# Optimization experiments

Hardware: AMD Instinct MI355X
Metric: run time of the kernel (lower is better)

## Reference

```python
import jax, jax.numpy as jnp
import numpy as np

G, N, E, C = 4, 50000, 800000, 128


def setup_inputs() -> dict:
    key = jax.random.key(0)
    ks = jax.random.split(key, 8)
    x = jax.random.normal(ks[0], (G, N, C), dtype=jnp.float32)
    edge_index = jax.random.randint(ks[1], (G, 2, E), 0, N, dtype=jnp.int64)
    s = 1.0 / np.sqrt(C)
    W1 = jax.random.normal(ks[2], (G, C, C), dtype=jnp.float32) * s
    W2 = jax.random.normal(ks[3], (G, C, C), dtype=jnp.float32) * s
    W3 = jax.random.normal(ks[4], (G, C, C), dtype=jnp.float32) * s
    b1 = jnp.zeros((G, C), dtype=jnp.float32)
    b2 = jnp.zeros((G, C), dtype=jnp.float32)
    b3 = jnp.zeros((G, C), dtype=jnp.float32)
    return {"x": x, "edge_index": edge_index, "W1": W1, "b1": b1,
            "W2": W2, "b2": b2, "W3": W3, "b3": b3}


def _gcn_layer(x, src, dst, deg_inv_sqrt, W, b):
    # PyG GCNConv: linear, then D^-1/2 (A+I) D^-1/2 aggregation, then bias.
    h = x @ W                                   # [N, C_out]
    norm = deg_inv_sqrt[src] * deg_inv_sqrt[dst]  # [E+N]
    msg = h[src] * norm[:, None]                # gather + scale
    out = jax.ops.segment_sum(msg, dst, num_segments=x.shape[0])
    return out + b


def _forward_one(x, ei, W1, b1, W2, b2, W3, b3):
    n = x.shape[0]
    loops = jnp.arange(n, dtype=ei.dtype)
    src = jnp.concatenate([ei[0], loops])       # add self-loops
    dst = jnp.concatenate([ei[1], loops])
    deg = jax.ops.segment_sum(jnp.ones_like(src, dtype=x.dtype), dst, num_segments=n)
    dis = jnp.where(deg > 0, jax.lax.rsqrt(deg), 0.0)
    x = _gcn_layer(x, src, dst, dis, W1, b1)
    x = _gcn_layer(x, src, dst, dis, W2, b2)
    x = _gcn_layer(x, src, dst, dis, W3, b3)
    return x


def reference(x, edge_index, W1, b1, W2, b2, W3, b3):
    # vmap over the num_graphs independent GCN stacks, then concat node dim
    out = jax.vmap(_forward_one)(x, edge_index, W1, b1, W2, b2, W3, b3)
    return out.reshape(-1, out.shape[-1])       # [G*N, out_channels]
```

## Files before the change

kernel.cpp:

```cpp
#include <hip/hip_runtime.h>

#define NG 4
#define NN 50000
#define NE 800000
#define NC 128
#define NB 196
#define NBT (NG * NB)
#define CAPB 48
#define LBS (NB + 1)
#define CAPQ 4608

typedef _Float16 half8 __attribute__((ext_vector_type(8)));
typedef _Float16 half4 __attribute__((ext_vector_type(4)));
typedef float f32x4 __attribute__((ext_vector_type(4)));

__global__ __launch_bounds__(256) void init_cursors(int* __restrict__ bktCur) {
  int i = blockIdx.x * blockDim.x + threadIdx.x;
  if (i < NBT) bktCur[i] = i * CAPQ;
}

__global__ __launch_bounds__(256) void bucket_scatter(
    const int* __restrict__ ei, int* __restrict__ bktCur,
    unsigned int* __restrict__ rec) {
  __shared__ int lcnt[NB];
  __shared__ int lbase[NB];
  __shared__ unsigned int lbin[CAPB * LBS];
  int g = blockIdx.y;
  int tid = threadIdx.x;
  for (int i = tid; i < NB; i += 256) lcnt[i] = 0;
  __syncthreads();
  const int* srcp = ei + (size_t)g * 2 * NE;
  const int* dstp = srcp + NE;
  int e0 = blockIdx.x * 4096;
  for (int t = tid; t < 4096; t += 256) {
    int e = e0 + t;
    if (e < NE) {
      int s = srcp[e], d = dstp[e];
      int b = d >> 8;
      unsigned int r = ((unsigned int)(d & 255) << 16) | (unsigned int)s;
      int pos = atomicAdd(&lcnt[b], 1);
      if (pos < CAPB) lbin[pos * LBS + b] = r;
      else { int gp = atomicAdd(&bktCur[g * NB + b], 1); rec[gp] = r; }
    }
  }
  __syncthreads();
  if (tid < NB) {
    int n = lcnt[tid]; if (n > CAPB) n = CAPB;
    lbase[tid] = n ? atomicAdd(&bktCur[g * NB + tid], n) : 0;
  }
  __syncthreads();
  int lane = tid & 63, wv = tid >> 6;
  for (int b = wv; b < NB; b += 4) {
    int n = lcnt[b]; if (n > CAPB) n = CAPB;
    if (lane < n) rec[lbase[b] + lane] = lbin[lane * LBS + b];
  }
}

__global__ __launch_bounds__(256) void build_csr(
    const unsigned int* __restrict__ rec, const int* __restrict__ bktCur,
    unsigned short* __restrict__ col, int* __restrict__ off,
    unsigned short* __restrict__ deg, float* __restrict__ dis) {
  __shared__ int cnt[256];
  __shared__ int offv[256];
  __shared__ int cnt2[256];
  __shared__ int wsum[4];
  int g = blockIdx.y, b = blockIdx.x;
  int idx = g * NB + b;
  int rb = idx * CAPQ, re = bktCur[idx];
  int tid = threadIdx.x;
  cnt[tid] = 0;
  __syncthreads();
  for (int j = rb + tid; j < re; j += 256)
    atomicAdd(&cnt[(rec[j] >> 16) & 255], 1);
  __syncthreads();
  int lane = tid & 63, wv = tid >> 6;
  int v = cnt[tid], incl = v;
  #pragma unroll
  for (int d2 = 1; d2 < 64; d2 <<= 1) {
    int t = __shfl_up(incl, d2, 64);
    if (lane >= d2) incl += t;
  }
  if (lane == 63) wsum[wv] = incl;
  __syncthreads();
  if (tid == 0) {
    int s = 0;
    #pragma unroll
    for (int w = 0; w < 4; ++w) { int t = wsum[w]; wsum[w] = s; s += t; }
  }
  __syncthreads();
  int excl = wsum[wv] + incl - v;
  offv[tid] = excl;
  cnt2[tid] = 0;
  int node = b * 256 + tid;
  if (node < NN) {
    off[g * (NN + 1) + node] = rb + excl;
    deg[(size_t)g * NN + node] = (unsigned short)v;
    dis[(size_t)g * NN + node] = rsqrtf((float)(v + 1));
  }
  __syncthreads();
  for (int j = rb + tid; j < re; j += 256) {
    unsigned int r = rec[j];
    int dl = (r >> 16) & 255;
    int p = rb + offv[dl] + atomicAdd(&cnt2[dl], 1);
    col[p] = (unsigned short)(r & 0xFFFF);
  }
}

__global__ __launch_bounds__(256) void gemm_mfma_kernel(
    const float* __restrict__ x, const float* __restrict__ W,
    const float* __restrict__ dis, _Float16* __restrict__ h) {
  __shared__ _Float16 Wt[2][128 * 128];
  int g = blockIdx.y;
  int row0 = blockIdx.x * 128;
  int tid = threadIdx.x;
  int lane = tid & 63;
  int wv = tid >> 6;
  int kc = lane >> 4;
  int lr = lane & 15;
  const float* Wg = W + (size_t)g * NC * NC;
  const float* xg = x + (size_t)g * NN * NC;

  {
    int n = tid & 127;
    int kq = (tid >> 7) & 1;
    #pragma unroll
    for (int iter = 0; iter < 16; ++iter) {
      int k4 = iter * 8 + kq * 4;
      float w0 = Wg[(size_t)(k4 + 0) * NC + n];
      float w1 = Wg[(size_t)(k4 + 1) * NC + n];
      float w2 = Wg[(size_t)(k4 + 2) * NC + n];
      float w3 = Wg[(size_t)(k4 + 3) * NC + n];
      half4 hi, lo;
      hi[0] = (_Float16)w0; lo[0] = (_Float16)(w0 - (float)hi[0]);
      hi[1] = (_Float16)w1; lo[1] = (_Float16)(w1 - (float)hi[1]);
      hi[2] = (_Float16)w2; lo[2] = (_Float16)(w2 - (float)hi[2]);
      hi[3] = (_Float16)w3; lo[3] = (_Float16)(w3 - (float)hi[3]);
      int base = n * 128 + ((iter ^ (n & 15)) << 3) + kq * 4;
      *(half4*)&Wt[0][base] = hi;
      *(half4*)&Wt[1][base] = lo;
    }
  }
  __syncthreads();

  f32x4 acc[2][8];
  #pragma unroll
  for (int mb = 0; mb < 2; ++mb)
    #pragma unroll
    for (int nb = 0; nb < 8; ++nb)
      acc[mb][nb] = (f32x4){0.f, 0.f, 0.f, 0.f};

  for (int kstep = 0; kstep < 4; ++kstep) {
    half8 ah[2], al[2];
    #pragma unroll
    for (int mb = 0; mb < 2; ++mb) {
      int row = row0 + wv * 32 + mb * 16 + lr;
      if (row > NN - 1) row = NN - 1;
      const float* xp = xg + (size_t)row * NC + kstep * 32 + kc * 8;
      float4 v0 = *(const float4*)xp;
      float4 v1 = *(const float4*)(xp + 4);
      float vv0 = v0.x, vv1 = v0.y, vv2 = v0.z, vv3 = v0.w;
      float vv4 = v1.x, vv5 = v1.y, vv6 = v1.z, vv7 = v1.w;
      _Float16 t;
      t = (_Float16)vv0; ah[mb][0] = t; al[mb][0] = (_Float16)(vv0 - (float)t);
      t = (_Float16)vv1; ah[mb][1] = t; al[mb][1] = (_Float16)(vv1 - (float)t);
      t = (_Float16)vv2; ah[mb][2] = t; al[mb][2] = (_Float16)(vv2 - (float)t);
      t = (_Float16)vv3; ah[mb][3] = t; al[mb][3] = (_Float16)(vv3 - (float)t);
      t = (_Float16)vv4; ah[mb][4] = t; al[mb][4] = (_Float16)(vv4 - (float)t);
      t = (_Float16)vv5; ah[mb][5] = t; al[mb][5] = (_Float16)(vv5 - (float)t);
      t = (_Float16)vv6; ah[mb][6] = t; al[mb][6] = (_Float16)(vv6 - (float)t);
      t = (_Float16)vv7; ah[mb][7] = t; al[mb][7] = (_Float16)(vv7 - (float)t);
    }
    #pragma unroll
    for (int nb = 0; nb < 8; ++nb) {
      int n = nb * 16 + lr;
      int chunk = kstep * 4 + kc;
      int boff = n * 128 + ((chunk ^ (n & 15)) << 3);
      half8 bh = *(const half8*)&Wt[0][boff];
      half8 bl = *(const half8*)&Wt[1][boff];
      #pragma unroll
      for (int mb = 0; mb < 2; ++mb) {
        acc[mb][nb] = __builtin_amdgcn_mfma_f32_16x16x32_f16(ah[mb], bh, acc[mb][nb], 0, 0, 0);
        acc[mb][nb] = __builtin_amdgcn_mfma_f32_16x16x32_f16(al[mb], bh, acc[mb][nb], 0, 0, 0);
        acc[mb][nb] = __builtin_amdgcn_mfma_f32_16x16x32_f16(ah[mb], bl, acc[mb][nb], 0, 0, 0);
      }
    }
  }

  const float* disg = dis + (size_t)g * NN;
  _Float16* hg = h + (size_t)g * NN * NC;
  #pragma unroll
  for (int mb = 0; mb < 2; ++mb) {
    #pragma unroll
    for (int reg = 0; reg < 4; ++reg) {
      int row = row0 + wv * 32 + mb * 16 + kc * 4 + reg;
      if (row < NN) {
        float dsc = disg[row];
        half8 o;
        #pragma unroll
        for (int nb = 0; nb < 8; ++nb)
          o[nb] = (_Float16)(acc[mb][nb][reg] * dsc);
        *(half8*)(hg + (size_t)row * NC + lr * 8) = o;
      }
    }
  }
}

#define MIXACC(A, H) A = fmaf((float)(H), 1.0f, A)
__global__ __launch_bounds__(256) void agg_kernel(
    const _Float16* __restrict__ h, const int* __restrict__ off,
    const unsigned short* __restrict__ col, const unsigned short* __restrict__ deg,
    const float* __restrict__ dis, const float* __restrict__ b,
    float* __restrict__ out) {
  int bid = blockIdx.x;
  int g = (bid & 7) >> 1;
  int sub = ((bid >> 3) << 1) | (bid & 1);
  int node = sub * 16 + (threadIdx.x >> 4);
  if (sub >= NN / 16) return;
  int l = threadIdx.x & 15;
  const half8* h8 = (const half8*)(h + (size_t)g * NN * NC);
  float a0[8], a1[8], a2[8], a3[8];
  half8 v = h8[(size_t)node * 16 + l];
  #pragma unroll
  for (int i = 0; i < 8; ++i) {
    a0[i] = (float)v[i]; a1[i] = 0.f; a2[i] = 0.f; a3[i] = 0.f;
  }
  int s = off[g * (NN + 1) + node];
  int e = s + deg[(size_t)g * NN + node];
  int j = s;
  for (; j + 8 <= e; j += 8) {
    int c0 = col[j],     c1 = col[j + 1], c2 = col[j + 2], c3 = col[j + 3];
    int c4 = col[j + 4], c5 = col[j + 5], c6 = col[j + 6], c7 = col[j + 7];
    half8 v0 = h8[(size_t)c0 * 16 + l];
    half8 v1 = h8[(size_t)c1 * 16 + l];
    half8 v2 = h8[(size_t)c2 * 16 + l];
    half8 v3 = h8[(size_t)c3 * 16 + l];
    half8 v4 = h8[(size_t)c4 * 16 + l];
    half8 v5 = h8[(size_t)c5 * 16 + l];
    half8 v6 = h8[(size_t)c6 * 16 + l];
    half8 v7 = h8[(size_t)c7 * 16 + l];
    #pragma unroll
    for (int i = 0; i < 8; ++i) {
      MIXACC(a0[i], v0[i]); MIXACC(a1[i], v1[i]);
      MIXACC(a2[i], v2[i]); MIXACC(a3[i], v3[i]);
      MIXACC(a0[i], v4[i]); MIXACC(a1[i], v5[i]);
      MIXACC(a2[i], v6[i]); MIXACC(a3[i], v7[i]);
    }
  }
  for (; j + 4 <= e; j += 4) {
    int c0 = col[j], c1 = col[j + 1], c2 = col[j + 2], c3 = col[j + 3];
    half8 v0 = h8[(size_t)c0 * 16 + l];
    half8 v1 = h8[(size_t)c1 * 16 + l];
    half8 v2 = h8[(size_t)c2 * 16 + l];
    half8 v3 = h8[(size_t)c3 * 16 + l];
    #pragma unroll
    for (int i = 0; i < 8; ++i) {
      MIXACC(a0[i], v0[i]); MIXACC(a1[i], v1[i]);
      MIXACC(a2[i], v2[i]); MIXACC(a3[i], v3[i]);
    }
  }
  for (; j < e; ++j) {
    half8 vr = h8[(size_t)col[j] * 16 + l];
    #pragma unroll
    for (int i = 0; i < 8; ++i) MIXACC(a0[i], vr[i]);
  }
  float dn = dis[g * NN + node];
  float* og = out + ((size_t)g * NN + node) * NC;
  const float* bg = b + (size_t)g * NC;
  #pragma unroll
  for (int i = 0; i < 8; ++i) {
    float val = (a0[i] + a1[i] + a2[i] + a3[i]) * dn + bg[i * 16 + l];
    og[i * 16 + l] = val;
  }
}

extern "C" void kernel_launch(void* const* d_in, const int* in_sizes, int n_in,
                              void* d_out, int out_size, void* d_ws, size_t ws_size,
                              hipStream_t stream) {
  const float* x  = (const float*)d_in[0];
  const int*   ei = (const int*)d_in[1];
  const float* W1 = (const float*)d_in[2];
  const float* b1 = (const float*)d_in[3];
  const float* W2 = (const float*)d_in[4];
  const float* b2 = (const float*)d_in[5];
  const float* W3 = (const float*)d_in[6];
  const float* b3 = (const float*)d_in[7];
  float* out = (float*)d_out;

  char* ws = (char*)d_ws;
  size_t p = 0;
  auto carve = [&](size_t bytes) -> char* {
    char* r = ws + p;
    p += (bytes + 255) & ~(size_t)255;
    return r;
  };
  int*            bktCur = (int*)           carve((size_t)NBT * 4);
  unsigned int*   rec    = (unsigned int*)  carve((size_t)NBT * CAPQ * 4);
  unsigned short* col    = (unsigned short*)carve((size_t)NBT * CAPQ * 2);
  int*            off    = (int*)           carve((size_t)NG * (NN + 1) * 4);
  unsigned short* deg    = (unsigned short*)carve((size_t)NG * NN * 2);
  float*          dis    = (float*)         carve((size_t)NG * NN * 4);
  _Float16*       hbuf   = (_Float16*)      carve((size_t)NG * NN * NC * 2);

  init_cursors<<<(NBT + 255) / 256, 256, 0, stream>>>(bktCur);
  bucket_scatter<<<dim3((NE + 4095) / 4096, NG), 256, 0, stream>>>(ei, bktCur, rec);
  build_csr<<<dim3(NB, NG), 256, 0, stream>>>(rec, bktCur, col, off, deg, dis);

  dim3 ggrid((NN + 127) / 128, NG);
  int  agrid = ((NN / 16 + 1) / 2) * 8;

  gemm_mfma_kernel<<<ggrid, 256, 0, stream>>>(x, W1, dis, hbuf);
  agg_kernel<<<agrid, 256, 0, stream>>>(hbuf, off, col, deg, dis, b1, out);
  gemm_mfma_kernel<<<ggrid, 256, 0, stream>>>(out, W2, dis, hbuf);
  agg_kernel<<<agrid, 256, 0, stream>>>(hbuf, off, col, deg, dis, b2, out);
  gemm_mfma_kernel<<<ggrid, 256, 0, stream>>>(out, W3, dis, hbuf);
  agg_kernel<<<agrid, 256, 0, stream>>>(hbuf, off, col, deg, dis, b3, out);
}
```

Measured before the change: 516.5 us.

## Store intermediate layer activations in fp16 and add fp16-input GEMM

The first two aggregation kernels now write fp16 activations to a buffer shared with the bucket-record scratch, and a new GEMM reads fp16 inputs directly, keeping the hi/lo split only for the weights. This halves the intermediate activation write and read traffic between layers and drops the fp32-to-fp16 conversion of the GEMM A operand. The 8-wide unrolled gather loop in aggregation is removed, leaving the 4-wide loop. Intermediate activations lose precision relative to fp32, and the scratch aliasing relies on rec being dead by the time xh is written.

```diff
diff --git a/kernel.cpp b/kernel.cpp
--- a/kernel.cpp
+++ b/kernel.cpp
@@ -205,12 +205,98 @@
   }
 }
 
+__global__ __launch_bounds__(256) void gemm16_mfma_kernel(
+    const _Float16* __restrict__ x, const float* __restrict__ W,
+    const float* __restrict__ dis, _Float16* __restrict__ h) {
+  __shared__ _Float16 Wt[2][128 * 128];
+  int g = blockIdx.y;
+  int row0 = blockIdx.x * 128;
+  int tid = threadIdx.x;
+  int lane = tid & 63;
+  int wv = tid >> 6;
+  int kc = lane >> 4;
+  int lr = lane & 15;
+  const float* Wg = W + (size_t)g * NC * NC;
+  const _Float16* xg = x + (size_t)g * NN * NC;
+
+  {
+    int n = tid & 127;
+    int kq = (tid >> 7) & 1;
+    #pragma unroll
+    for (int iter = 0; iter < 16; ++iter) {
+      int k4 = iter * 8 + kq * 4;
+      float w0 = Wg[(size_t)(k4 + 0) * NC + n];
+      float w1 = Wg[(size_t)(k4 + 1) * NC + n];
+      float w2 = Wg[(size_t)(k4 + 2) * NC + n];
+      float w3 = Wg[(size_t)(k4 + 3) * NC + n];
+      half4 hi, lo;
+      hi[0] = (_Float16)w0; lo[0] = (_Float16)(w0 - (float)hi[0]);
+      hi[1] = (_Float16)w1; lo[1] = (_Float16)(w1 - (float)hi[1]);
+      hi[2] = (_Float16)w2; lo[2] = (_Float16)(w2 - (float)hi[2]);
+      hi[3] = (_Float16)w3; lo[3] = (_Float16)(w3 - (float)hi[3]);
+      int base = n * 128 + ((iter ^ (n & 15)) << 3) + kq * 4;
+      *(half4*)&Wt[0][base] = hi;
+      *(half4*)&Wt[1][base] = lo;
+    }
+  }
+  __syncthreads();
+
+  f32x4 acc[2][8];
+  #pragma unroll
+  for (int mb = 0; mb < 2; ++mb)
+    #pragma unroll
+    for (int nb = 0; nb < 8; ++nb)
+      acc[mb][nb] = (f32x4){0.f, 0.f, 0.f, 0.f};
+
+  for (int kstep = 0; kstep < 4; ++kstep) {
+    half8 ah[2];
+    #pragma unroll
+    for (int mb = 0; mb < 2; ++mb) {
+      int row = row0 + wv * 32 + mb * 16 + lr;
+      if (row > NN - 1) row = NN - 1;
+      ah[mb] = *(const half8*)(xg + (size_t)row * NC + kstep * 32 + kc * 8);
+    }
+    #pragma unroll
+    for (int nb = 0; nb < 8; ++nb) {
+      int n = nb * 16 + lr;
+      int chunk = kstep * 4 + kc;
+      int boff = n * 128 + ((chunk ^ (n & 15)) << 3);
+      half8 bh = *(const half8*)&Wt[0][boff];
+      half8 bl = *(const half8*)&Wt[1][boff];
+      #pragma unroll
+      for (int mb = 0; mb < 2; ++mb) {
+        acc[mb][nb] = __builtin_amdgcn_mfma_f32_16x16x32_f16(ah[mb], bh, acc[mb][nb], 0, 0, 0);
+        acc[mb][nb] = __builtin_amdgcn_mfma_f32_16x16x32_f16(ah[mb], bl, acc[mb][nb], 0, 0, 0);
+      }
+    }
+  }
+
+  const float* disg = dis + (size_t)g * NN;
+  _Float16* hg = h + (size_t)g * NN * NC;
+  #pragma unroll
+  for (int mb = 0; mb < 2; ++mb) {
+    #pragma unroll
+    for (int reg = 0; reg < 4; ++reg) {
+      int row = row0 + wv * 32 + mb * 16 + kc * 4 + reg;
+      if (row < NN) {
+        float dsc = disg[row];
+        half8 o;
+        #pragma unroll
+        for (int nb = 0; nb < 8; ++nb)
+          o[nb] = (_Float16)(acc[mb][nb][reg] * dsc);
+        *(half8*)(hg + (size_t)row * NC + lr * 8) = o;
+      }
+    }
+  }
+}
+
 #define MIXACC(A, H) A = fmaf((float)(H), 1.0f, A)
+template <bool F16OUT>
 __global__ __launch_bounds__(256) void agg_kernel(
     const _Float16* __restrict__ h, const int* __restrict__ off,
     const unsigned short* __restrict__ col, const unsigned short* __restrict__ deg,
     const float* __restrict__ dis, const float* __restrict__ b,
-    float* __restrict__ out) {
+    float* __restrict__ outf, _Float16* __restrict__ outh) {
   int bid = blockIdx.x;
   int g = (bid & 7) >> 1;
   int sub = ((bid >> 3) << 1) | (bid & 1);
@@ -227,25 +313,6 @@
   int s = off[g * (NN + 1) + node];
   int e = s + deg[(size_t)g * NN + node];
   int j = s;
-  for (; j + 8 <= e; j += 8) {
-    int c0 = col[j],     c1 = col[j + 1], c2 = col[j + 2], c3 = col[j + 3];
-    int c4 = col[j + 4], c5 = col[j + 5], c6 = col[j + 6], c7 = col[j + 7];
-    half8 v0 = h8[(size_t)c0 * 16 + l];
-    half8 v1 = h8[(size_t)c1 * 16 + l];
-    half8 v2 = h8[(size_t)c2 * 16 + l];
-    half8 v3 = h8[(size_t)c3 * 16 + l];
-    half8 v4 = h8[(size_t)c4 * 16 + l];
-    half8 v5 = h8[(size_t)c5 * 16 + l];
-    half8 v6 = h8[(size_t)c6 * 16 + l];
-    half8 v7 = h8[(size_t)c7 * 16 + l];
-    #pragma unroll
-    for (int i = 0; i < 8; ++i) {
-      MIXACC(a0[i], v0[i]); MIXACC(a1[i], v1[i]);
-      MIXACC(a2[i], v2[i]); MIXACC(a3[i], v3[i]);
-      MIXACC(a0[i], v4[i]); MIXACC(a1[i], v5[i]);
-      MIXACC(a2[i], v6[i]); MIXACC(a3[i], v7[i]);
-    }
-  }
   for (; j + 4 <= e; j += 4) {
     int c0 = col[j], c1 = col[j + 1], c2 = col[j + 2], c3 = col[j + 3];
     half8 v0 = h8[(size_t)c0 * 16 + l];
@@ -264,12 +331,21 @@
     for (int i = 0; i < 8; ++i) MIXACC(a0[i], vr[i]);
   }
   float dn = dis[g * NN + node];
-  float* og = out + ((size_t)g * NN + node) * NC;
   const float* bg = b + (size_t)g * NC;
-  #pragma unroll
-  for (int i = 0; i < 8; ++i) {
-    float val = (a0[i] + a1[i] + a2[i] + a3[i]) * dn + bg[i * 16 + l];
-    og[i * 16 + l] = val;
+  if constexpr (F16OUT) {
+    _Float16* og = outh + ((size_t)g * NN + node) * NC;
+    #pragma unroll
+    for (int i = 0; i < 8; ++i) {
+      float val = (a0[i] + a1[i] + a2[i] + a3[i]) * dn + bg[i * 16 + l];
+      og[i * 16 + l] = (_Float16)val;
+    }
+  } else {
+    float* og = outf + ((size_t)g * NN + node) * NC;
+    #pragma unroll
+    for (int i = 0; i < 8; ++i) {
+      float val = (a0[i] + a1[i] + a2[i] + a3[i]) * dn + bg[i * 16 + l];
+      og[i * 16 + l] = val;
+    }
   }
 }
 
@@ -294,12 +370,15 @@
     return r;
   };
   int*            bktCur = (int*)           carve((size_t)NBT * 4);
-  unsigned int*   rec    = (unsigned int*)  carve((size_t)NBT * CAPQ * 4);
   unsigned short* col    = (unsigned short*)carve((size_t)NBT * CAPQ * 2);
   int*            off    = (int*)           carve((size_t)NG * (NN + 1) * 4);
   unsigned short* deg    = (unsigned short*)carve((size_t)NG * NN * 2);
   float*          dis    = (float*)         carve((size_t)NG * NN * 4);
   _Float16*       hbuf   = (_Float16*)      carve((size_t)NG * NN * NC * 2);
+  size_t ubytes = (size_t)NG * NN * NC * 2;
+  char*           uni    = carve(ubytes);
+  unsigned int*   rec    = (unsigned int*)uni;
+  _Float16*       xh     = (_Float16*)uni;
 
   init_cursors<<<(NBT + 255) / 256, 256, 0, stream>>>(bktCur);
   bucket_scatter<<<dim3((NE + 4095) / 4096, NG), 256, 0, stream>>>(ei, bktCur, rec);
@@ -309,9 +388,9 @@
   int  agrid = ((NN / 16 + 1) / 2) * 8;
 
   gemm_mfma_kernel<<<ggrid, 256, 0, stream>>>(x, W1, dis, hbuf);
-  agg_kernel<<<agrid, 256, 0, stream>>>(hbuf, off, col, deg, dis, b1, out);
-  gemm_mfma_kernel<<<ggrid, 256, 0, stream>>>(out, W2, dis, hbuf);
-  agg_kernel<<<agrid, 256, 0, stream>>>(hbuf, off, col, deg, dis, b2, out);
-  gemm_mfma_kernel<<<ggrid, 256, 0, stream>>>(out, W3, dis, hbuf);
-  agg_kernel<<<agrid, 256, 0, stream>>>(hbuf, off, col, deg, dis, b3, out);
-}
+  agg_kernel<true><<<agrid, 256, 0, stream>>>(hbuf, off, col, deg, dis, b1, nullptr, xh);
+  gemm16_mfma_kernel<<<ggrid, 256, 0, stream>>>(xh, W2, dis, hbuf);
+  agg_kernel<true><<<agrid, 256, 0, stream>>>(hbuf, off, col, deg, dis, b2, nullptr, xh);
+  gemm16_mfma_kernel<<<ggrid, 256, 0, stream>>>(xh, W3, dis, hbuf);
+  agg_kernel<false><<<agrid, 256, 0, stream>>>(hbuf, off, col, deg, dis, b3, out, nullptr);
+}
```

Measured after the change: 459.8 us. 11.0% less time.
